# Kernel optimization log

Measured on AMD Instinct MI355X. Metric: run time of the kernel, lower is better.

The kernel has to match this reference:

```python
import jax, jax.numpy as jnp
import numpy as np

# dims
B, L = 2, 1024            # batch, seq len (queries == keys)
DQ, DK, DSRC = 1024, 1024, 512
VIEWS, WIDTH, TOPK = 8, 4, 8
DVP = DQ // VIEWS         # per-view head dim = 128
PAD_F = (WIDTH - 1) // 2  # dilocal 'same' zero padding (stride=1, dilation=1)
PAD_B = (WIDTH - 1) - PAD_F


def setup_inputs() -> dict:
    key = jax.random.key(0)
    ks = jax.random.split(key, 5)
    s = 0.02
    return {
        "query": jax.random.normal(ks[0], (B, L, DQ), jnp.float32),
        "key_t": jax.random.normal(ks[1], (B, L, DK), jnp.float32),
        "source": jax.random.normal(ks[2], (B, L, DSRC), jnp.float32),
        "wq": jax.random.normal(ks[3], (VIEWS, DVP, DQ), jnp.float32) * s,
        "bq": jnp.zeros((VIEWS, DVP), jnp.float32),
        "wk": jax.random.normal(ks[4], (VIEWS, DVP, DK), jnp.float32) * s,
        "bk": jnp.zeros((VIEWS, DVP), jnp.float32),
    }


def reference(query, key_t, source, wq, bq, wk, bk):
    # --- ViewPointFactory.forward ---
    # multi-view projections: [B, L, D] -> [B, views, L, dvp]
    q = jnp.einsum('bld,vkd->bvlk', query, wq) + bq[None, :, None, :]
    k = jnp.einsum('bld,vkd->bvlk', key_t, wk) + bk[None, :, None, :]
    # attention scores over all keys: [B, views, Lq, Lk] (no sqrt(d) scaling in source)
    score = jnp.einsum('bvqd,bvkd->bvqk', q, k)
    # torch.sort(descending) + slice == top_k with sorted values
    vals, idx = jax.lax.top_k(score, TOPK)          # [B, views, Lq, TOPK]
    weights = jax.nn.softmax(vals, axis=-1)

    # --- ViewPoint.__call__(source) ---
    # dilocal: width-WIDTH local windows, stride 1, dilation 1, zero 'same' pad
    padded = jnp.pad(source, ((0, 0), (PAD_F, PAD_B), (0, 0)))
    win_idx = jnp.arange(L)[:, None] + jnp.arange(WIDTH)[None, :]  # [L, WIDTH]
    windows = padded[:, win_idx, :]                 # [B, L, WIDTH, DSRC]

    # gather the top-k key windows per (view, query): [B, views, Lq, TOPK, WIDTH, DSRC]
    gathered = jax.vmap(lambda w, i: w[i])(windows, idx)
    # weighted sum over top-k -> [B, views, Lq, WIDTH, DSRC]
    out = jnp.einsum('bvqk,bvqkwd->bvqwd', weights, gathered)
    return out
```

## Files before the change

### kernel.cpp

```cpp
#include <hip/hip_runtime.h>
#include <cstdint>

#define L_SEQ 1024
#define DSRC 512
#define XPL 2097152L
#define WPL 1048576L

typedef __attribute__((ext_vector_type(8))) short short8;
typedef __attribute__((ext_vector_type(4))) float floatx4;

__device__ __forceinline__ unsigned short f2bf(float f) {
  unsigned int x = __float_as_uint(f);
  x += 0x7fff + ((x >> 16) & 1);
  return (unsigned short)(x >> 16);
}
__device__ __forceinline__ float bf2f(unsigned short h) {
  return __uint_as_float((unsigned)h << 16);
}
__device__ __forceinline__ void split3(float f, unsigned short* h) {
  h[0] = f2bf(f);
  float d = f - bf2f(h[0]);
  h[1] = f2bf(d);
  h[2] = f2bf(d - bf2f(h[1]));
}

__global__ __launch_bounds__(256) void split_inputs_k(
    const float* __restrict__ query, const float* __restrict__ key_t,
    const float* __restrict__ wq, const float* __restrict__ wk,
    ushort* __restrict__ xs, ushort* __restrict__ wsp) {
  int blk = blockIdx.x;
  const float* in; ushort* out; long pl; int idx;
  if (blk < 2048)      { in = query; out = xs;           pl = XPL; idx = blk; }
  else if (blk < 4096) { in = key_t; out = xs + 3 * XPL; pl = XPL; idx = blk - 2048; }
  else if (blk < 5120) { in = wq;    out = wsp;          pl = WPL; idx = blk - 4096; }
  else                 { in = wk;    out = wsp + 3 * WPL; pl = WPL; idx = blk - 5120; }
  long e = (long)idx * 1024 + threadIdx.x * 4;
  float4 v = *(const float4*)(in + e);
  unsigned short h0[3], h1[3], h2[3], h3[3];
  split3(v.x, h0); split3(v.y, h1); split3(v.z, h2); split3(v.w, h3);
#pragma unroll
  for (int s = 0; s < 3; s++) {
    ushort4 u; u.x = h0[s]; u.y = h1[s]; u.z = h2[s]; u.w = h3[s];
    *(ushort4*)(out + s * pl + e) = u;
  }
}

__global__ __launch_bounds__(512) void proj_gemm_k(
    const ushort* __restrict__ xs, const ushort* __restrict__ wsp,
    float* __restrict__ C, const float* __restrict__ bq, const float* __restrict__ bk) {
  __shared__ ushort As[3][4096];
  __shared__ ushort Bs[3][4096];
  int z = blockIdx.z;
  const ushort* Ab = xs + (long)z * 3 * XPL + (long)blockIdx.y * 128 * 1024;
  const ushort* Bb = wsp + (long)z * 3 * WPL + (long)blockIdx.x * 128 * 1024;
  const float* bias = z ? bk : bq;

  int tid = threadIdx.x;
  int lane = tid & 63, wv = tid >> 6;
  int wm = wv >> 2, wn = wv & 3;
  int quad = lane >> 4, l16 = lane & 15;

  int sr = tid >> 2;
  int sc = (tid & 3) * 8;

  floatx4 acc[4][2] = {};

  for (int k0 = 0; k0 < 1024; k0 += 32) {
    short8 ga[3], gb[3];
#pragma unroll
    for (int s = 0; s < 3; s++) {
      ga[s] = *(const short8*)(Ab + s * XPL + (long)sr * 1024 + k0 + sc);
      gb[s] = *(const short8*)(Bb + s * WPL + (long)sr * 1024 + k0 + sc);
    }
    __syncthreads();
#pragma unroll
    for (int s = 0; s < 3; s++) {
      *(short8*)(&As[s][sr * 32 + sc]) = ga[s];
      *(short8*)(&Bs[s][sr * 32 + sc]) = gb[s];
    }
    __syncthreads();

    short8 af[3][4];
#pragma unroll
    for (int s = 0; s < 3; s++)
#pragma unroll
      for (int i = 0; i < 4; i++)
        af[s][i] = *(const short8*)(&As[s][(wm * 64 + i * 16 + l16) * 32 + quad * 8]);
#pragma unroll
    for (int j = 0; j < 2; j++) {
      int boff = (wn * 32 + j * 16 + l16) * 32 + quad * 8;
      short8 b0 = *(const short8*)(&Bs[0][boff]);
      short8 b1 = *(const short8*)(&Bs[1][boff]);
      short8 b2 = *(const short8*)(&Bs[2][boff]);
#pragma unroll
      for (int i = 0; i < 4; i++) {
        acc[i][j] = __builtin_amdgcn_mfma_f32_16x16x32_bf16(af[1][i], b1, acc[i][j], 0, 0, 0);
        acc[i][j] = __builtin_amdgcn_mfma_f32_16x16x32_bf16(af[0][i], b2, acc[i][j], 0, 0, 0);
        acc[i][j] = __builtin_amdgcn_mfma_f32_16x16x32_bf16(af[2][i], b0, acc[i][j], 0, 0, 0);
        acc[i][j] = __builtin_amdgcn_mfma_f32_16x16x32_bf16(af[0][i], b1, acc[i][j], 0, 0, 0);
        acc[i][j] = __builtin_amdgcn_mfma_f32_16x16x32_bf16(af[1][i], b0, acc[i][j], 0, 0, 0);
        acc[i][j] = __builtin_amdgcn_mfma_f32_16x16x32_bf16(af[0][i], b0, acc[i][j], 0, 0, 0);
      }
    }
  }

  float* Cb = C + (long)z * XPL;
#pragma unroll
  for (int j = 0; j < 2; j++) {
    int col = blockIdx.x * 128 + wn * 32 + j * 16 + l16;
    float bv = bias[col];
#pragma unroll
    for (int i = 0; i < 4; i++) {
#pragma unroll
      for (int r = 0; r < 4; r++) {
        int row = blockIdx.y * 128 + wm * 64 + i * 16 + quad * 4 + r;
        Cb[(long)row * 1024 + col] = acc[i][j][r] + bv;
      }
    }
  }
}

__global__ __launch_bounds__(256) void score_gemm_k(
    const float* __restrict__ qp, const float* __restrict__ kp,
    float* __restrict__ S) {
  __shared__ ushort As[3][4096];
  __shared__ ushort Bs[3][4096];
  int z = blockIdx.z;
  int b = z >> 3, v = z & 7;
  const float* Aq = qp + (long)b * 1048576 + v * 128 + (long)blockIdx.y * 128 * 1024;
  const float* Bq = kp + (long)b * 1048576 + v * 128 + (long)blockIdx.x * 128 * 1024;

  int tid = threadIdx.x;
  int lane = tid & 63, wv = tid >> 6;
  int wm = wv >> 1, wn = wv & 1;
  int quad = lane >> 4, l16 = lane & 15;

  int sr = tid >> 3;
  int sc4 = (tid & 7) * 4;

  floatx4 acc[4][4] = {};

  for (int k0 = 0; k0 < 128; k0 += 32) {
    float4 av[4], bv4[4];
#pragma unroll
    for (int it = 0; it < 4; it++) {
      av[it] = *(const float4*)(Aq + (long)(sr + 32 * it) * 1024 + k0 + sc4);
      bv4[it] = *(const float4*)(Bq + (long)(sr + 32 * it) * 1024 + k0 + sc4);
    }
    __syncthreads();
#pragma unroll
    for (int it = 0; it < 4; it++) {
      int r = sr + 32 * it;
      const float* afp = (const float*)&av[it];
      const float* bfp = (const float*)&bv4[it];
      unsigned short ha[4][3], hb[4][3];
#pragma unroll
      for (int e = 0; e < 4; e++) { split3(afp[e], ha[e]); split3(bfp[e], hb[e]); }
#pragma unroll
      for (int s = 0; s < 3; s++) {
        ushort4 ua; ua.x = ha[0][s]; ua.y = ha[1][s]; ua.z = ha[2][s]; ua.w = ha[3][s];
        ushort4 ub; ub.x = hb[0][s]; ub.y = hb[1][s]; ub.z = hb[2][s]; ub.w = hb[3][s];
        *(ushort4*)(&As[s][r * 32 + sc4]) = ua;
        *(ushort4*)(&Bs[s][r * 32 + sc4]) = ub;
      }
    }
    __syncthreads();

    short8 af[3][4];
#pragma unroll
    for (int s = 0; s < 3; s++)
#pragma unroll
      for (int i = 0; i < 4; i++)
        af[s][i] = *(const short8*)(&As[s][(wm * 64 + i * 16 + l16) * 32 + quad * 8]);
#pragma unroll
    for (int j = 0; j < 4; j++) {
      int boff = (wn * 64 + j * 16 + l16) * 32 + quad * 8;
      short8 b0 = *(const short8*)(&Bs[0][boff]);
      short8 b1 = *(const short8*)(&Bs[1][boff]);
      short8 b2 = *(const short8*)(&Bs[2][boff]);
#pragma unroll
      for (int i = 0; i < 4; i++) {
        acc[i][j] = __builtin_amdgcn_mfma_f32_16x16x32_bf16(af[1][i], b1, acc[i][j], 0, 0, 0);
        acc[i][j] = __builtin_amdgcn_mfma_f32_16x16x32_bf16(af[0][i], b2, acc[i][j], 0, 0, 0);
        acc[i][j] = __builtin_amdgcn_mfma_f32_16x16x32_bf16(af[2][i], b0, acc[i][j], 0, 0, 0);
        acc[i][j] = __builtin_amdgcn_mfma_f32_16x16x32_bf16(af[0][i], b1, acc[i][j], 0, 0, 0);
        acc[i][j] = __builtin_amdgcn_mfma_f32_16x16x32_bf16(af[1][i], b0, acc[i][j], 0, 0, 0);
        acc[i][j] = __builtin_amdgcn_mfma_f32_16x16x32_bf16(af[0][i], b0, acc[i][j], 0, 0, 0);
      }
    }
  }

  float* Sb = S + (long)z * 1048576;
#pragma unroll
  for (int j = 0; j < 4; j++) {
    int col = blockIdx.x * 128 + wn * 64 + j * 16 + l16;
#pragma unroll
    for (int i = 0; i < 4; i++) {
#pragma unroll
      for (int r = 0; r < 4; r++) {
        int row = blockIdx.y * 128 + wm * 64 + i * 16 + quad * 4 + r;
        Sb[(long)row * 1024 + col] = acc[i][j][r];
      }
    }
  }
}

__global__ __launch_bounds__(256) void topk_softmax_k(const float* __restrict__ scores,
                                                      float* __restrict__ wts,
                                                      int* __restrict__ idxs) {
  int row = blockIdx.x * 4 + (threadIdx.x >> 6);
  int lane = threadIdx.x & 63;
  const float* s = scores + (long)row * 1024;
  float v[16];
#pragma unroll
  for (int i = 0; i < 16; i++) v[i] = s[lane + i * 64];

  float topv[8]; int topi[8];
  for (int t = 0; t < 8; t++) {
    float bv = -1e30f; int bi = 1 << 30; int bslot = -1;
#pragma unroll
    for (int i = 0; i < 16; i++) {
      int ci = lane + i * 64;
      if (v[i] > bv) { bv = v[i]; bi = ci; bslot = i; }
    }
    float rv = bv; int ri = bi;
    for (int off = 32; off; off >>= 1) {
      float ov = __shfl_down(rv, off);
      int oi = __shfl_down(ri, off);
      if (ov > rv || (ov == rv && oi < ri)) { rv = ov; ri = oi; }
    }
    rv = __shfl(rv, 0); ri = __shfl(ri, 0);
    topv[t] = rv; topi[t] = ri;
    if (bslot >= 0 && bi == ri) v[bslot] = -1e30f;
  }
  float m = topv[0], sum = 0.f, e[8];
#pragma unroll
  for (int t = 0; t < 8; t++) { e[t] = __expf(topv[t] - m); sum += e[t]; }
  float inv = 1.0f / sum;
  if (lane < 8) {
    wts[(long)row * 8 + lane] = e[lane] * inv;
    idxs[(long)row * 8 + lane] = topi[lane];
  }
}

__global__ __launch_bounds__(256) void gather_out_k(const float* __restrict__ src,
                                                    const float* __restrict__ wts,
                                                    const int* __restrict__ idxs,
                                                    float* __restrict__ out) {
  int rowid = blockIdx.x;
  int b = rowid >> 13;
  int tid = threadIdx.x;
  int d4 = tid & 127;
  int w0 = (tid >> 7) << 1;
  const float4* s4 = (const float4*)src + (long)b * (L_SEQ * (DSRC / 4));
  float wt[8]; int id[8];
#pragma unroll
  for (int k = 0; k < 8; k++) {
    wt[k] = wts[(long)rowid * 8 + k];
    id[k] = idxs[(long)rowid * 8 + k];
  }
  float ax = 0, ay = 0, az = 0, aw = 0;
  float bx = 0, by = 0, bz2 = 0, bw = 0;
#pragma unroll
  for (int k = 0; k < 8; k++) {
    int r0 = id[k] + w0 - 1;
    if ((unsigned)r0 < (unsigned)L_SEQ) {
      float4 x = s4[(long)r0 * 128 + d4];
      ax += wt[k] * x.x; ay += wt[k] * x.y; az += wt[k] * x.z; aw += wt[k] * x.w;
    }
    int r1 = r0 + 1;
    if ((unsigned)r1 < (unsigned)L_SEQ) {
      float4 x = s4[(long)r1 * 128 + d4];
      bx += wt[k] * x.x; by += wt[k] * x.y; bz2 += wt[k] * x.z; bw += wt[k] * x.w;
    }
  }
  float4* o4 = (float4*)out + ((long)rowid * 4 + w0) * 128 + d4;
  o4[0] = make_float4(ax, ay, az, aw);
  o4[128] = make_float4(bx, by, bz2, bw);
}

extern "C" void kernel_launch(void* const* d_in, const int* in_sizes, int n_in,
                              void* d_out, int out_size, void* d_ws, size_t ws_size,
                              hipStream_t stream) {
  (void)in_sizes; (void)n_in; (void)out_size; (void)ws_size;
  const float* query  = (const float*)d_in[0];
  const float* key_t  = (const float*)d_in[1];
  const float* source = (const float*)d_in[2];
  const float* wq     = (const float*)d_in[3];
  const float* bq     = (const float*)d_in[4];
  const float* wk     = (const float*)d_in[5];
  const float* bk     = (const float*)d_in[6];

  char* ws = (char*)d_ws;
  float* qp   = (float*)(ws + 0);
  float* kp   = (float*)(ws + 8388608);
  float* wts  = (float*)(ws + 16777216);
  int*   idxs = (int*)(ws + 17301504);
  ushort* xs  = (ushort*)(ws + 17825792);
  ushort* wsp = (ushort*)(ws + 17825792 + 25165824);
  float* sc   = (float*)(ws + 17825792);

  split_inputs_k<<<6144, 256, 0, stream>>>(query, key_t, wq, wk, xs, wsp);
  proj_gemm_k<<<dim3(8, 16, 2), 512, 0, stream>>>(xs, wsp, qp, bq, bk);
  score_gemm_k<<<dim3(8, 8, 16), 256, 0, stream>>>(qp, kp, sc);
  topk_softmax_k<<<4096, 256, 0, stream>>>(sc, wts, idxs);
  gather_out_k<<<16384, 256, 0, stream>>>(source, wts, idxs, (float*)d_out);
}
```

Measured before the change: 320.2 us.

## Pipeline projection GEMM with direct-to-LDS loads and emit pre-split bf16 projections

The projection GEMM now uses global_load_lds with an XOR-swizzled LDS layout and double buffering, so the next K tile loads while MFMAs run. Its epilogue writes the projections already split into three bf16 planes, which removes the per-tile split3 work and the fp32 loads in the score GEMM. The score GEMM moves to 512 threads with the same direct-to-LDS loads and runs once per batch, each pass followed by its own top-k pass, which keeps the score buffer small and cache-resident. Top-k reads rows as float4 with remapped column indices. Costs are more LDS per block, more launches, and stores of 3-plane ushort output in the projection epilogue.

```diff
diff --git a/kernel.cpp b/kernel.cpp
--- a/kernel.cpp
+++ b/kernel.cpp
@@ -22,6 +22,12 @@
   float d = f - bf2f(h[0]);
   h[1] = f2bf(d);
   h[2] = f2bf(d - bf2f(h[1]));
+}
+
+__device__ __forceinline__ void gload_lds16(const void* g, void* l) {
+  __builtin_amdgcn_global_load_lds(
+      (const __attribute__((address_space(1))) unsigned int*)g,
+      (__attribute__((address_space(3))) unsigned int*)l, 16, 0, 0);
 }
 
 __global__ __launch_bounds__(256) void split_inputs_k(
@@ -45,15 +51,15 @@
   }
 }
 
-__global__ __launch_bounds__(512) void proj_gemm_k(
+__global__ __launch_bounds__(512, 2) void proj_gemm_k(
     const ushort* __restrict__ xs, const ushort* __restrict__ wsp,
-    float* __restrict__ C, const float* __restrict__ bq, const float* __restrict__ bk) {
-  __shared__ ushort As[3][4096];
-  __shared__ ushort Bs[3][4096];
+    ushort* __restrict__ qs, ushort* __restrict__ ks,
+    const float* __restrict__ bq, const float* __restrict__ bk) {
+  __shared__ ushort As[2][3][4096];
+  __shared__ ushort Bs[2][3][4096];
   int z = blockIdx.z;
   const ushort* Ab = xs + (long)z * 3 * XPL + (long)blockIdx.y * 128 * 1024;
   const ushort* Bb = wsp + (long)z * 3 * WPL + (long)blockIdx.x * 128 * 1024;
-  const float* bias = z ? bk : bq;
 
   int tid = threadIdx.x;
   int lane = tid & 63, wv = tid >> 6;
@@ -61,37 +67,44 @@
   int quad = lane >> 4, l16 = lane & 15;
 
   int sr = tid >> 2;
-  int sc = (tid & 3) * 8;
+  int scq = (((tid & 3) ^ ((sr >> 1) & 3)) << 3);
 
   floatx4 acc[4][2] = {};
 
-  for (int k0 = 0; k0 < 1024; k0 += 32) {
-    short8 ga[3], gb[3];
-#pragma unroll
-    for (int s = 0; s < 3; s++) {
-      ga[s] = *(const short8*)(Ab + s * XPL + (long)sr * 1024 + k0 + sc);
-      gb[s] = *(const short8*)(Bb + s * WPL + (long)sr * 1024 + k0 + sc);
-    }
-    __syncthreads();
-#pragma unroll
-    for (int s = 0; s < 3; s++) {
-      *(short8*)(&As[s][sr * 32 + sc]) = ga[s];
-      *(short8*)(&Bs[s][sr * 32 + sc]) = gb[s];
-    }
-    __syncthreads();
-
+#pragma unroll
+  for (int s = 0; s < 3; s++) {
+    gload_lds16(Ab + (long)s * XPL + (long)sr * 1024 + scq, &As[0][s][wv * 512]);
+    gload_lds16(Bb + (long)s * WPL + (long)sr * 1024 + scq, &Bs[0][s][wv * 512]);
+  }
+  __syncthreads();
+
+  int cur = 0;
+#pragma unroll 2
+  for (int t = 0; t < 32; t++) {
+    if (t < 31) {
+      int k0 = (t + 1) * 32;
+#pragma unroll
+      for (int s = 0; s < 3; s++) {
+        gload_lds16(Ab + (long)s * XPL + (long)sr * 1024 + k0 + scq, &As[cur ^ 1][s][wv * 512]);
+        gload_lds16(Bb + (long)s * WPL + (long)sr * 1024 + k0 + scq, &Bs[cur ^ 1][s][wv * 512]);
+      }
+    }
     short8 af[3][4];
 #pragma unroll
     for (int s = 0; s < 3; s++)
 #pragma unroll
-      for (int i = 0; i < 4; i++)
-        af[s][i] = *(const short8*)(&As[s][(wm * 64 + i * 16 + l16) * 32 + quad * 8]);
+      for (int i = 0; i < 4; i++) {
+        int row = wm * 64 + i * 16 + l16;
+        int qa = (quad ^ ((row >> 1) & 3)) << 3;
+        af[s][i] = *(const short8*)(&As[cur][s][row * 32 + qa]);
+      }
 #pragma unroll
     for (int j = 0; j < 2; j++) {
-      int boff = (wn * 32 + j * 16 + l16) * 32 + quad * 8;
-      short8 b0 = *(const short8*)(&Bs[0][boff]);
-      short8 b1 = *(const short8*)(&Bs[1][boff]);
-      short8 b2 = *(const short8*)(&Bs[2][boff]);
+      int rowb = wn * 32 + j * 16 + l16;
+      int boff = rowb * 32 + ((quad ^ ((rowb >> 1) & 3)) << 3);
+      short8 b0 = *(const short8*)(&Bs[cur][0][boff]);
+      short8 b1 = *(const short8*)(&Bs[cur][1][boff]);
+      short8 b2 = *(const short8*)(&Bs[cur][2][boff]);
 #pragma unroll
       for (int i = 0; i < 4; i++) {
         acc[i][j] = __builtin_amdgcn_mfma_f32_16x16x32_bf16(af[1][i], b1, acc[i][j], 0, 0, 0);
@@ -102,9 +115,12 @@
         acc[i][j] = __builtin_amdgcn_mfma_f32_16x16x32_bf16(af[0][i], b0, acc[i][j], 0, 0, 0);
       }
     }
-  }
-
-  float* Cb = C + (long)z * XPL;
+    __syncthreads();
+    cur ^= 1;
+  }
+
+  ushort* Ob = z ? ks : qs;
+  const float* bias = z ? bk : bq;
 #pragma unroll
   for (int j = 0; j < 2; j++) {
     int col = blockIdx.x * 128 + wn * 32 + j * 16 + l16;
@@ -113,68 +129,58 @@
     for (int i = 0; i < 4; i++) {
 #pragma unroll
       for (int r = 0; r < 4; r++) {
-        int row = blockIdx.y * 128 + wm * 64 + i * 16 + quad * 4 + r;
-        Cb[(long)row * 1024 + col] = acc[i][j][r] + bv;
-      }
-    }
-  }
-}
-
-__global__ __launch_bounds__(256) void score_gemm_k(
-    const float* __restrict__ qp, const float* __restrict__ kp,
-    float* __restrict__ S) {
+        long row = blockIdx.y * 128 + wm * 64 + i * 16 + quad * 4 + r;
+        float val = acc[i][j][r] + bv;
+        unsigned short h[3]; split3(val, h);
+        long e = row * 1024 + col;
+#pragma unroll
+        for (int s = 0; s < 3; s++) Ob[s * XPL + e] = h[s];
+      }
+    }
+  }
+}
+
+__global__ __launch_bounds__(512, 4) void score_gemm_k(
+    const ushort* __restrict__ qs, const ushort* __restrict__ ks,
+    float* __restrict__ S, int b) {
   __shared__ ushort As[3][4096];
   __shared__ ushort Bs[3][4096];
-  int z = blockIdx.z;
-  int b = z >> 3, v = z & 7;
-  const float* Aq = qp + (long)b * 1048576 + v * 128 + (long)blockIdx.y * 128 * 1024;
-  const float* Bq = kp + (long)b * 1048576 + v * 128 + (long)blockIdx.x * 128 * 1024;
+  int v = blockIdx.z;
+  const ushort* Ab = qs + (long)b * 1048576 + v * 128 + (long)blockIdx.y * 131072;
+  const ushort* Bb = ks + (long)b * 1048576 + v * 128 + (long)blockIdx.x * 131072;
 
   int tid = threadIdx.x;
   int lane = tid & 63, wv = tid >> 6;
-  int wm = wv >> 1, wn = wv & 1;
+  int wm = wv >> 2, wn = wv & 3;
   int quad = lane >> 4, l16 = lane & 15;
 
-  int sr = tid >> 3;
-  int sc4 = (tid & 7) * 4;
-
-  floatx4 acc[4][4] = {};
-
-  for (int k0 = 0; k0 < 128; k0 += 32) {
-    float4 av[4], bv4[4];
-#pragma unroll
-    for (int it = 0; it < 4; it++) {
-      av[it] = *(const float4*)(Aq + (long)(sr + 32 * it) * 1024 + k0 + sc4);
-      bv4[it] = *(const float4*)(Bq + (long)(sr + 32 * it) * 1024 + k0 + sc4);
+  int sr = tid >> 2;
+  int scq = (((tid & 3) ^ ((sr >> 1) & 3)) << 3);
+
+  floatx4 acc[4][2] = {};
+
+  for (int t = 0; t < 4; t++) {
+    int k0 = t * 32;
+#pragma unroll
+    for (int s = 0; s < 3; s++) {
+      gload_lds16(Ab + (long)s * XPL + (long)sr * 1024 + k0 + scq, &As[s][wv * 512]);
+      gload_lds16(Bb + (long)s * XPL + (long)sr * 1024 + k0 + scq, &Bs[s][wv * 512]);
     }
     __syncthreads();
-#pragma unroll
-    for (int it = 0; it < 4; it++) {
-      int r = sr + 32 * it;
-      const float* afp = (const float*)&av[it];
-      const float* bfp = (const float*)&bv4[it];
-      unsigned short ha[4][3], hb[4][3];
-#pragma unroll
-      for (int e = 0; e < 4; e++) { split3(afp[e], ha[e]); split3(bfp[e], hb[e]); }
-#pragma unroll
-      for (int s = 0; s < 3; s++) {
-        ushort4 ua; ua.x = ha[0][s]; ua.y = ha[1][s]; ua.z = ha[2][s]; ua.w = ha[3][s];
-        ushort4 ub; ub.x = hb[0][s]; ub.y = hb[1][s]; ub.z = hb[2][s]; ub.w = hb[3][s];
-        *(ushort4*)(&As[s][r * 32 + sc4]) = ua;
-        *(ushort4*)(&Bs[s][r * 32 + sc4]) = ub;
-      }
-    }
-    __syncthreads();
 
     short8 af[3][4];
 #pragma unroll
     for (int s = 0; s < 3; s++)
 #pragma unroll
-      for (int i = 0; i < 4; i++)
-        af[s][i] = *(const short8*)(&As[s][(wm * 64 + i * 16 + l16) * 32 + quad * 8]);
-#pragma unroll
-    for (int j = 0; j < 4; j++) {
-      int boff = (wn * 64 + j * 16 + l16) * 32 + quad * 8;
+      for (int i = 0; i < 4; i++) {
+        int row = wm * 64 + i * 16 + l16;
+        int qa = (quad ^ ((row >> 1) & 3)) << 3;
+        af[s][i] = *(const short8*)(&As[s][row * 32 + qa]);
+      }
+#pragma unroll
+    for (int j = 0; j < 2; j++) {
+      int rowb = wn * 32 + j * 16 + l16;
+      int boff = rowb * 32 + ((quad ^ ((rowb >> 1) & 3)) << 3);
       short8 b0 = *(const short8*)(&Bs[0][boff]);
       short8 b1 = *(const short8*)(&Bs[1][boff]);
       short8 b2 = *(const short8*)(&Bs[2][boff]);
@@ -188,12 +194,13 @@
         acc[i][j] = __builtin_amdgcn_mfma_f32_16x16x32_bf16(af[0][i], b0, acc[i][j], 0, 0, 0);
       }
     }
-  }
-
-  float* Sb = S + (long)z * 1048576;
-#pragma unroll
-  for (int j = 0; j < 4; j++) {
-    int col = blockIdx.x * 128 + wn * 64 + j * 16 + l16;
+    __syncthreads();
+  }
+
+  float* Sb = S + (long)v * 1048576;
+#pragma unroll
+  for (int j = 0; j < 2; j++) {
+    int col = blockIdx.x * 128 + wn * 32 + j * 16 + l16;
 #pragma unroll
     for (int i = 0; i < 4; i++) {
 #pragma unroll
@@ -210,17 +217,19 @@
                                                       int* __restrict__ idxs) {
   int row = blockIdx.x * 4 + (threadIdx.x >> 6);
   int lane = threadIdx.x & 63;
-  const float* s = scores + (long)row * 1024;
+  const float4* s4 = (const float4*)(scores + (long)row * 1024);
   float v[16];
 #pragma unroll
-  for (int i = 0; i < 16; i++) v[i] = s[lane + i * 64];
-
+  for (int i = 0; i < 4; i++) {
+    float4 t4 = s4[i * 64 + lane];
+    v[i * 4 + 0] = t4.x; v[i * 4 + 1] = t4.y; v[i * 4 + 2] = t4.z; v[i * 4 + 3] = t4.w;
+  }
   float topv[8]; int topi[8];
   for (int t = 0; t < 8; t++) {
     float bv = -1e30f; int bi = 1 << 30; int bslot = -1;
 #pragma unroll
     for (int i = 0; i < 16; i++) {
-      int ci = lane + i * 64;
+      int ci = ((i >> 2) << 8) + (lane << 2) + (i & 3);
       if (v[i] > bv) { bv = v[i]; bi = ci; bslot = i; }
     }
     float rv = bv; int ri = bi;
@@ -292,17 +301,19 @@
   const float* bk     = (const float*)d_in[6];
 
   char* ws = (char*)d_ws;
-  float* qp   = (float*)(ws + 0);
-  float* kp   = (float*)(ws + 8388608);
-  float* wts  = (float*)(ws + 16777216);
-  int*   idxs = (int*)(ws + 17301504);
-  ushort* xs  = (ushort*)(ws + 17825792);
-  ushort* wsp = (ushort*)(ws + 17825792 + 25165824);
-  float* sc   = (float*)(ws + 17825792);
+  ushort* qs  = (ushort*)(ws);
+  ushort* ksp = (ushort*)(ws + 12582912);
+  float*  wts = (float*)(ws + 25165824);
+  int*    idxs= (int*)(ws + 25690112);
+  ushort* xs  = (ushort*)(ws + 26214400);
+  ushort* wsp = (ushort*)(ws + 51380224);
+  float*  sc  = (float*)(ws + 26214400);
 
   split_inputs_k<<<6144, 256, 0, stream>>>(query, key_t, wq, wk, xs, wsp);
-  proj_gemm_k<<<dim3(8, 16, 2), 512, 0, stream>>>(xs, wsp, qp, bq, bk);
-  score_gemm_k<<<dim3(8, 8, 16), 256, 0, stream>>>(qp, kp, sc);
-  topk_softmax_k<<<4096, 256, 0, stream>>>(sc, wts, idxs);
+  proj_gemm_k<<<dim3(8, 16, 2), 512, 0, stream>>>(xs, wsp, qs, ksp, bq, bk);
+  for (int b = 0; b < 2; b++) {
+    score_gemm_k<<<dim3(8, 8, 8), 512, 0, stream>>>(qs, ksp, sc, b);
+    topk_softmax_k<<<2048, 256, 0, stream>>>(sc, wts + (long)b * 65536, idxs + b * 65536);
+  }
   gather_out_k<<<16384, 256, 0, stream>>>(source, wts, idxs, (float*)d_out);
 }
```

Result: slower. 328.8 us (+2.7%).
